# Kernel tuning notes

Measured on AMD Instinct MI355X. Metric: run time of the kernel, lower is better.

The kernel has to match this reference:

```python
import jax, jax.numpy as jnp
import numpy as np

H = 1024      # hidden_dim
E = 512       # word_emb_dim
A = 512       # av_emb_dim
L = 512       # max_length
V = 50257     # n_vocab


def setup_inputs() -> dict:
    key = jax.random.key(0)
    ks = jax.random.split(key, 16)
    s = lambda k, shape, scale=0.02: (jax.random.normal(k, shape, dtype=jnp.float32) * scale)
    return {
        "word": jax.random.randint(ks[0], (1,), 0, V),
        "enc_seq_len": 1,
        "av_emb": s(ks[1], (1, A), 1.0),
        "h0": s(ks[2], (1, 1, H), 1.0),
        "c0": s(ks[3], (1, 1, H), 1.0),
        "encoder_outputs": s(ks[4], (L, H), 1.0),
        "emb_table": s(ks[5], (V, E)),
        "attn_W": s(ks[6], (L, E + H)),
        "attn_b": s(ks[7], (L,)),
        "comb_W": s(ks[8], (H, E + H + A)),
        "comb_b": s(ks[9], (H,)),
        "W_ih": s(ks[10], (4 * H, H)),
        "W_hh": s(ks[11], (4 * H, H)),
        "b_ih": s(ks[12], (4 * H,)),
        "b_hh": s(ks[13], (4 * H,)),
        "out_W": s(ks[14], (V, H)),
        "out_b": s(ks[15], (V,)),
    }


def reference(word, enc_seq_len, av_emb, h0, c0, encoder_outputs,
              emb_table, attn_W, attn_b, comb_W, comb_b,
              W_ih, W_hh, b_ih, b_hh, out_W, out_b):
    # embedded: [1, E]
    embedded = emb_table[word].reshape(1, -1)
    h = h0[0]  # [1, H]
    c = c0[0]  # [1, H]

    # attention scores over encoder positions: [1, L]
    attn_pre = jnp.concatenate([embedded, h], axis=1) @ attn_W.T + attn_b
    # faithful to original: rows >= enc_seq_len set to -inf (no-op for batch dim of 1 when enc_seq_len>=1)
    row = jnp.arange(attn_pre.shape[0])[:, None]
    attn_pre = jnp.where(row >= enc_seq_len, -jnp.inf, attn_pre)
    attn_weights = jax.nn.softmax(attn_pre, axis=1)           # [1, L]
    attn_applied = attn_weights @ encoder_outputs             # [1, H]

    # combine + relu: [1, H]
    comb = jnp.concatenate([embedded, attn_applied, av_emb], axis=1)
    x = jax.nn.relu(comb @ comb_W.T + comb_b)

    # single-step LSTM (torch gate order: i, f, g, o)
    gates = x @ W_ih.T + b_ih + h @ W_hh.T + b_hh             # [1, 4H]
    i, f, g, o = jnp.split(gates, 4, axis=1)
    c_new = jax.nn.sigmoid(f) * c + jax.nn.sigmoid(i) * jnp.tanh(g)
    h_new = jax.nn.sigmoid(o) * jnp.tanh(c_new)

    logits = h_new @ out_W.T + out_b                          # [1, V]
    return logits, h_new[None], c_new[None], attn_weights
```

## Files before the change

### kernel.cpp

```cpp
#include <hip/hip_runtime.h>
#include <hip/hip_bf16.h>


#define WS_CAT1   0
#define WS_COMB   1536
#define WS_PRE    3584
#define WS_ATTNW  4096
#define WS_X      4608
#define WS_GATES  5632
#define WS_HNEW   9728

#define OUT_H     50257
#define OUT_C     51281
#define OUT_AW    52305

__device__ __forceinline__ float wave_partial_dot(const float* __restrict__ Wrow,
                                                  const float* __restrict__ x,
                                                  int cols) {
  int lane = threadIdx.x & 63;
  float acc = 0.f;
  for (int c = lane * 4; c < cols; c += 256) {
    float4 w  = *reinterpret_cast<const float4*>(Wrow + c);
    float4 xv = *reinterpret_cast<const float4*>(x + c);
    acc += w.x * xv.x + w.y * xv.y + w.z * xv.z + w.w * xv.w;
  }
  return acc;
}

__device__ __forceinline__ float wave_reduce(float acc) {
#pragma unroll
  for (int off = 32; off > 0; off >>= 1) acc += __shfl_xor(acc, off, 64);
  return acc;
}

__global__ __launch_bounds__(1024) void prep_k(const int* __restrict__ word,
                                               const float* __restrict__ emb_table,
                                               const float* __restrict__ h0,
                                               const float* __restrict__ av,
                                               float* __restrict__ ws) {
  int t = threadIdx.x;
  int w = word[0];
  if (t < 512) {
    float e = emb_table[(size_t)w * 512 + t];
    ws[WS_CAT1 + t] = e;
    ws[WS_COMB + t] = e;
    ws[WS_COMB + 1536 + t] = av[t];
  }
  ws[WS_CAT1 + 512 + t] = h0[t];
}

template <int COLS, bool RELU>
__global__ __launch_bounds__(256) void matvec_k(const float* __restrict__ W,
                                                const float* __restrict__ bias,
                                                const float* __restrict__ x,
                                                float* __restrict__ y,
                                                int rows) {
  int row = blockIdx.x * 4 + (threadIdx.x >> 6);
  if (row >= rows) return;
  float acc = wave_partial_dot(W + (size_t)row * COLS, x, COLS);
  acc = wave_reduce(acc);
  if ((threadIdx.x & 63) == 0) {
    acc += bias[row];
    if (RELU) acc = fmaxf(acc, 0.f);
    y[row] = acc;
  }
}

__global__ __launch_bounds__(512) void softmax_k(const float* __restrict__ pre,
                                                 float* __restrict__ wout,
                                                 float* __restrict__ out_w) {
  __shared__ float red[8];
  __shared__ float stat[2];
  int t = threadIdx.x;
  int lane = t & 63, wid = t >> 6;
  float v = pre[t];
  float m = v;
#pragma unroll
  for (int off = 32; off > 0; off >>= 1) m = fmaxf(m, __shfl_xor(m, off, 64));
  if (lane == 0) red[wid] = m;
  __syncthreads();
  if (t == 0) {
    float mm = red[0];
    for (int i = 1; i < 8; i++) mm = fmaxf(mm, red[i]);
    stat[0] = mm;
  }
  __syncthreads();
  float e = expf(v - stat[0]);
  float s = e;
#pragma unroll
  for (int off = 32; off > 0; off >>= 1) s += __shfl_xor(s, off, 64);
  if (lane == 0) red[wid] = s;
  __syncthreads();
  if (t == 0) {
    float ss = 0.f;
    for (int i = 0; i < 8; i++) ss += red[i];
    stat[1] = ss;
  }
  __syncthreads();
  float w = e / stat[1];
  wout[t] = w;
  out_w[t] = w;
}

__global__ __launch_bounds__(256) void attn_apply_k(const float* __restrict__ w,
                                                    const float* __restrict__ enc,
                                                    float* __restrict__ out) {
  int j = blockIdx.x * 256 + threadIdx.x;
  float a0 = 0.f, a1 = 0.f, a2 = 0.f, a3 = 0.f;
  for (int l = 0; l < 512; l += 4) {
    a0 += w[l + 0] * enc[(size_t)(l + 0) * 1024 + j];
    a1 += w[l + 1] * enc[(size_t)(l + 1) * 1024 + j];
    a2 += w[l + 2] * enc[(size_t)(l + 2) * 1024 + j];
    a3 += w[l + 3] * enc[(size_t)(l + 3) * 1024 + j];
  }
  out[j] = (a0 + a1) + (a2 + a3);
}

__global__ __launch_bounds__(256) void gates_k(const float* __restrict__ Wih,
                                               const float* __restrict__ Whh,
                                               const float* __restrict__ bih,
                                               const float* __restrict__ bhh,
                                               const float* __restrict__ x,
                                               const float* __restrict__ h,
                                               float* __restrict__ g) {
  int row = blockIdx.x * 4 + (threadIdx.x >> 6);
  float acc = wave_partial_dot(Wih + (size_t)row * 1024, x, 1024) +
              wave_partial_dot(Whh + (size_t)row * 1024, h, 1024);
  acc = wave_reduce(acc);
  if ((threadIdx.x & 63) == 0) g[row] = acc + bih[row] + bhh[row];
}

__global__ __launch_bounds__(1024) void lstm_k(const float* __restrict__ g,
                                               const float* __restrict__ c0,
                                               float* __restrict__ hnew_f,
                                               float* __restrict__ out_h,
                                               float* __restrict__ out_c) {
  int t = threadIdx.x;
  float gi = g[t], gf = g[1024 + t], gg = g[2048 + t], go = g[3072 + t];
  float i = 1.f / (1.f + expf(-gi));
  float f = 1.f / (1.f + expf(-gf));
  float gt = tanhf(gg);
  float o = 1.f / (1.f + expf(-go));
  float cn = f * c0[t] + i * gt;
  float hn = o * tanhf(cn);
  hnew_f[t] = hn;
  out_h[t] = hn;
  out_c[t] = cn;
}

template <int COLS>
__global__ __launch_bounds__(256) void matvec_out_k(const float* __restrict__ W,
                                                    const float* __restrict__ bias,
                                                    const float* __restrict__ x,
                                                    float* __restrict__ y,
                                                    int rows) {
  int row = blockIdx.x * 4 + (threadIdx.x >> 6);
  if (row >= rows) return;
  float acc = wave_partial_dot(W + (size_t)row * COLS, x, COLS);
  acc = wave_reduce(acc);
  if ((threadIdx.x & 63) == 0) {
    y[row] = acc + bias[row];
  }
}

extern "C" void kernel_launch(void* const* d_in, const int* in_sizes, int n_in,
                              void* d_out, int out_size, void* d_ws, size_t ws_size,
                              hipStream_t stream) {
  const int*   word   = (const int*)  d_in[0];
  const float* av     = (const float*)d_in[2];
  const float* h0     = (const float*)d_in[3];
  const float* c0     = (const float*)d_in[4];
  const float* enc    = (const float*)d_in[5];
  const float* emb    = (const float*)d_in[6];
  const float* attn_W = (const float*)d_in[7];
  const float* attn_b = (const float*)d_in[8];
  const float* comb_W = (const float*)d_in[9];
  const float* comb_b = (const float*)d_in[10];
  const float* W_ih   = (const float*)d_in[11];
  const float* W_hh   = (const float*)d_in[12];
  const float* b_ih   = (const float*)d_in[13];
  const float* b_hh   = (const float*)d_in[14];
  const float* out_W  = (const float*)d_in[15];
  const float* out_b  = (const float*)d_in[16];

  float* ws  = (float*)d_ws;
  float* out = (float*)d_out;

  prep_k<<<1, 1024, 0, stream>>>(word, emb, h0, av, ws);
  matvec_k<1536, false><<<128, 256, 0, stream>>>(attn_W, attn_b,
      ws + WS_CAT1, ws + WS_PRE, 512);
  softmax_k<<<1, 512, 0, stream>>>(ws + WS_PRE, ws + WS_ATTNW, out + OUT_AW);
  attn_apply_k<<<4, 256, 0, stream>>>(ws + WS_ATTNW, enc, ws + WS_COMB + 512);
  matvec_k<2048, true><<<256, 256, 0, stream>>>(comb_W, comb_b,
      ws + WS_COMB, ws + WS_X, 1024);
  gates_k<<<1024, 256, 0, stream>>>(W_ih, W_hh, b_ih, b_hh,
      ws + WS_X, ws + WS_CAT1 + 512, ws + WS_GATES);
  lstm_k<<<1, 1024, 0, stream>>>(ws + WS_GATES, c0,
      ws + WS_HNEW, out + OUT_H, out + OUT_C);
  matvec_out_k<1024><<<(50257 + 3) / 4, 256, 0, stream>>>(out_W, out_b,
      ws + WS_HNEW, out, 50257);
}
```

Baseline: 417.6 us.

## Fuse decoder kernels and split attention-apply over positions with atomics

Removes the prep kernel by reading the embedding row and h0 directly inside the attention and combine matvecs. The LSTM nonlinearity is fused into the gates kernel by assigning one block per hidden unit, with its four gate rows on four waves. The attention-apply step is split across 32 blocks that combine partial sums with atomics into a buffer zeroed by softmax. The logits matvec now computes two rows per wave to reuse the loaded input vector. Together these cut kernel launches and raise parallelism in the small attention-apply step, at the cost of atomic accumulation order being nondeterministic.

```diff
diff --git a/kernel.cpp b/kernel.cpp
--- a/kernel.cpp
+++ b/kernel.cpp
@@ -1,78 +1,67 @@
 #include <hip/hip_runtime.h>
-#include <hip/hip_bf16.h>
-
-
-#define WS_CAT1   0
-#define WS_COMB   1536
-#define WS_PRE    3584
-#define WS_ATTNW  4096
-#define WS_X      4608
-#define WS_GATES  5632
-#define WS_HNEW   9728
+
+
+#define V 50257
+
+#define WS_PRE    0
+#define WS_ATTNW  512
+#define WS_APPL   1024
+#define WS_X      2048
 
 #define OUT_H     50257
 #define OUT_C     51281
 #define OUT_AW    52305
 
-__device__ __forceinline__ float wave_partial_dot(const float* __restrict__ Wrow,
-                                                  const float* __restrict__ x,
-                                                  int cols) {
+__device__ __forceinline__ float4 ld4(const float* p) {
+  return *reinterpret_cast<const float4*>(p);
+}
+__device__ __forceinline__ float dot4(float4 a, float4 b) {
+  return a.x * b.x + a.y * b.y + a.z * b.z + a.w * b.w;
+}
+__device__ __forceinline__ float wave_reduce(float a) {
+#pragma unroll
+  for (int off = 32; off > 0; off >>= 1) a += __shfl_xor(a, off, 64);
+  return a;
+}
+__device__ __forceinline__ float sigf(float v) {
+  return 1.f / (1.f + expf(-v));
+}
+
+__global__ __launch_bounds__(256) void attn_mv_k(const float* __restrict__ attn_W,
+                                                 const float* __restrict__ attn_b,
+                                                 const float* __restrict__ emb,
+                                                 const int* __restrict__ word,
+                                                 const float* __restrict__ h0,
+                                                 float* __restrict__ pre) {
+  int row = blockIdx.x * 4 + (threadIdx.x >> 6);
   int lane = threadIdx.x & 63;
-  float acc = 0.f;
-  for (int c = lane * 4; c < cols; c += 256) {
-    float4 w  = *reinterpret_cast<const float4*>(Wrow + c);
-    float4 xv = *reinterpret_cast<const float4*>(x + c);
-    acc += w.x * xv.x + w.y * xv.y + w.z * xv.z + w.w * xv.w;
-  }
-  return acc;
-}
-
-__device__ __forceinline__ float wave_reduce(float acc) {
-#pragma unroll
-  for (int off = 32; off > 0; off >>= 1) acc += __shfl_xor(acc, off, 64);
-  return acc;
-}
-
-__global__ __launch_bounds__(1024) void prep_k(const int* __restrict__ word,
-                                               const float* __restrict__ emb_table,
-                                               const float* __restrict__ h0,
-                                               const float* __restrict__ av,
-                                               float* __restrict__ ws) {
-  int t = threadIdx.x;
-  int w = word[0];
-  if (t < 512) {
-    float e = emb_table[(size_t)w * 512 + t];
-    ws[WS_CAT1 + t] = e;
-    ws[WS_COMB + t] = e;
-    ws[WS_COMB + 1536 + t] = av[t];
-  }
-  ws[WS_CAT1 + 512 + t] = h0[t];
-}
-
-template <int COLS, bool RELU>
-__global__ __launch_bounds__(256) void matvec_k(const float* __restrict__ W,
-                                                const float* __restrict__ bias,
-                                                const float* __restrict__ x,
-                                                float* __restrict__ y,
-                                                int rows) {
-  int row = blockIdx.x * 4 + (threadIdx.x >> 6);
-  if (row >= rows) return;
-  float acc = wave_partial_dot(W + (size_t)row * COLS, x, COLS);
+  const float* Wr = attn_W + (size_t)row * 1536;
+  const float* er = emb + (size_t)word[0] * 512;
+  float acc = 0.f;
+#pragma unroll
+  for (int k = 0; k < 2; k++) {
+    int c = lane * 4 + k * 256;
+    acc += dot4(ld4(Wr + c), ld4(er + c));
+  }
+#pragma unroll
+  for (int k = 2; k < 6; k++) {
+    int c = lane * 4 + k * 256;
+    acc += dot4(ld4(Wr + c), ld4(h0 + c - 512));
+  }
   acc = wave_reduce(acc);
-  if ((threadIdx.x & 63) == 0) {
-    acc += bias[row];
-    if (RELU) acc = fmaxf(acc, 0.f);
-    y[row] = acc;
-  }
+  if (lane == 0) pre[row] = acc + attn_b[row];
 }
 
 __global__ __launch_bounds__(512) void softmax_k(const float* __restrict__ pre,
                                                  float* __restrict__ wout,
-                                                 float* __restrict__ out_w) {
+                                                 float* __restrict__ out_w,
+                                                 float* __restrict__ applied) {
   __shared__ float red[8];
   __shared__ float stat[2];
   int t = threadIdx.x;
   int lane = t & 63, wid = t >> 6;
+  applied[t] = 0.f;
+  applied[512 + t] = 0.f;
   float v = pre[t];
   float m = v;
 #pragma unroll
@@ -104,62 +93,106 @@
 
 __global__ __launch_bounds__(256) void attn_apply_k(const float* __restrict__ w,
                                                     const float* __restrict__ enc,
-                                                    float* __restrict__ out) {
-  int j = blockIdx.x * 256 + threadIdx.x;
-  float a0 = 0.f, a1 = 0.f, a2 = 0.f, a3 = 0.f;
-  for (int l = 0; l < 512; l += 4) {
-    a0 += w[l + 0] * enc[(size_t)(l + 0) * 1024 + j];
-    a1 += w[l + 1] * enc[(size_t)(l + 1) * 1024 + j];
-    a2 += w[l + 2] * enc[(size_t)(l + 2) * 1024 + j];
-    a3 += w[l + 3] * enc[(size_t)(l + 3) * 1024 + j];
-  }
-  out[j] = (a0 + a1) + (a2 + a3);
-}
-
-__global__ __launch_bounds__(256) void gates_k(const float* __restrict__ Wih,
-                                               const float* __restrict__ Whh,
-                                               const float* __restrict__ bih,
-                                               const float* __restrict__ bhh,
-                                               const float* __restrict__ x,
-                                               const float* __restrict__ h,
-                                               float* __restrict__ g) {
+                                                    float* __restrict__ applied) {
+  int jb = blockIdx.x & 3, lb = blockIdx.x >> 2;
+  int j = jb * 256 + threadIdx.x;
+  int l0 = lb * 64;
+  float acc = 0.f;
+#pragma unroll 4
+  for (int l = l0; l < l0 + 64; l++) acc += w[l] * enc[(size_t)l * 1024 + j];
+  atomicAdd(applied + j, acc);
+}
+
+__global__ __launch_bounds__(256) void comb_mv_k(const float* __restrict__ comb_W,
+                                                 const float* __restrict__ comb_b,
+                                                 const float* __restrict__ emb,
+                                                 const int* __restrict__ word,
+                                                 const float* __restrict__ applied,
+                                                 const float* __restrict__ av,
+                                                 float* __restrict__ x) {
   int row = blockIdx.x * 4 + (threadIdx.x >> 6);
-  float acc = wave_partial_dot(Wih + (size_t)row * 1024, x, 1024) +
-              wave_partial_dot(Whh + (size_t)row * 1024, h, 1024);
+  int lane = threadIdx.x & 63;
+  const float* Wr = comb_W + (size_t)row * 2048;
+  const float* er = emb + (size_t)word[0] * 512;
+  float acc = 0.f;
+#pragma unroll
+  for (int k = 0; k < 2; k++) {
+    int c = lane * 4 + k * 256;
+    acc += dot4(ld4(Wr + c), ld4(er + c));
+  }
+#pragma unroll
+  for (int k = 2; k < 6; k++) {
+    int c = lane * 4 + k * 256;
+    acc += dot4(ld4(Wr + c), ld4(applied + c - 512));
+  }
+#pragma unroll
+  for (int k = 6; k < 8; k++) {
+    int c = lane * 4 + k * 256;
+    acc += dot4(ld4(Wr + c), ld4(av + c - 1536));
+  }
   acc = wave_reduce(acc);
-  if ((threadIdx.x & 63) == 0) g[row] = acc + bih[row] + bhh[row];
-}
-
-__global__ __launch_bounds__(1024) void lstm_k(const float* __restrict__ g,
-                                               const float* __restrict__ c0,
-                                               float* __restrict__ hnew_f,
-                                               float* __restrict__ out_h,
-                                               float* __restrict__ out_c) {
-  int t = threadIdx.x;
-  float gi = g[t], gf = g[1024 + t], gg = g[2048 + t], go = g[3072 + t];
-  float i = 1.f / (1.f + expf(-gi));
-  float f = 1.f / (1.f + expf(-gf));
-  float gt = tanhf(gg);
-  float o = 1.f / (1.f + expf(-go));
-  float cn = f * c0[t] + i * gt;
-  float hn = o * tanhf(cn);
-  hnew_f[t] = hn;
-  out_h[t] = hn;
-  out_c[t] = cn;
-}
-
-template <int COLS>
-__global__ __launch_bounds__(256) void matvec_out_k(const float* __restrict__ W,
-                                                    const float* __restrict__ bias,
+  if (lane == 0) x[row] = fmaxf(acc + comb_b[row], 0.f);
+}
+
+__global__ __launch_bounds__(256) void gates_lstm_k(const float* __restrict__ Wih,
+                                                    const float* __restrict__ Whh,
+                                                    const float* __restrict__ bih,
+                                                    const float* __restrict__ bhh,
                                                     const float* __restrict__ x,
-                                                    float* __restrict__ y,
-                                                    int rows) {
-  int row = blockIdx.x * 4 + (threadIdx.x >> 6);
-  if (row >= rows) return;
-  float acc = wave_partial_dot(W + (size_t)row * COLS, x, COLS);
+                                                    const float* __restrict__ h0,
+                                                    const float* __restrict__ c0,
+                                                    float* __restrict__ out_h,
+                                                    float* __restrict__ out_c) {
+  __shared__ float gsh[4];
+  int t = blockIdx.x;
+  int wv = threadIdx.x >> 6, lane = threadIdx.x & 63;
+  size_t r = (size_t)wv * 1024 + t;
+  const float* Wi = Wih + r * 1024;
+  const float* Wh = Whh + r * 1024;
+  float acc = 0.f;
+#pragma unroll
+  for (int k = 0; k < 4; k++) {
+    int c = lane * 4 + k * 256;
+    acc += dot4(ld4(Wi + c), ld4(x + c));
+    acc += dot4(ld4(Wh + c), ld4(h0 + c));
+  }
   acc = wave_reduce(acc);
-  if ((threadIdx.x & 63) == 0) {
-    y[row] = acc + bias[row];
+  if (lane == 0) gsh[wv] = acc + bih[r] + bhh[r];
+  __syncthreads();
+  if (threadIdx.x == 0) {
+    float gi = sigf(gsh[0]);
+    float gf = sigf(gsh[1]);
+    float gg = tanhf(gsh[2]);
+    float go = sigf(gsh[3]);
+    float cn = gf * c0[t] + gi * gg;
+    float hn = go * tanhf(cn);
+    out_h[t] = hn;
+    out_c[t] = cn;
+  }
+}
+
+__global__ __launch_bounds__(256) void logits_mv_k(const float* __restrict__ W,
+                                                   const float* __restrict__ bias,
+                                                   const float* __restrict__ x,
+                                                   float* __restrict__ y) {
+  int wv = threadIdx.x >> 6, lane = threadIdx.x & 63;
+  int r0 = blockIdx.x * 8 + wv * 2;
+  if (r0 >= V) return;
+  bool has1 = (r0 + 1) < V;
+  const float* W0 = W + (size_t)r0 * 1024;
+  float a0 = 0.f, a1 = 0.f;
+#pragma unroll
+  for (int k = 0; k < 4; k++) {
+    int c = lane * 4 + k * 256;
+    float4 xv = ld4(x + c);
+    a0 += dot4(ld4(W0 + c), xv);
+    if (has1) a1 += dot4(ld4(W0 + 1024 + c), xv);
+  }
+  a0 = wave_reduce(a0);
+  a1 = wave_reduce(a1);
+  if (lane == 0) {
+    y[r0] = a0 + bias[r0];
+    if (has1) y[r0 + 1] = a1 + bias[r0 + 1];
   }
 }
 
@@ -186,17 +219,13 @@
   float* ws  = (float*)d_ws;
   float* out = (float*)d_out;
 
-  prep_k<<<1, 1024, 0, stream>>>(word, emb, h0, av, ws);
-  matvec_k<1536, false><<<128, 256, 0, stream>>>(attn_W, attn_b,
-      ws + WS_CAT1, ws + WS_PRE, 512);
-  softmax_k<<<1, 512, 0, stream>>>(ws + WS_PRE, ws + WS_ATTNW, out + OUT_AW);
-  attn_apply_k<<<4, 256, 0, stream>>>(ws + WS_ATTNW, enc, ws + WS_COMB + 512);
-  matvec_k<2048, true><<<256, 256, 0, stream>>>(comb_W, comb_b,
-      ws + WS_COMB, ws + WS_X, 1024);
-  gates_k<<<1024, 256, 0, stream>>>(W_ih, W_hh, b_ih, b_hh,
-      ws + WS_X, ws + WS_CAT1 + 512, ws + WS_GATES);
-  lstm_k<<<1, 1024, 0, stream>>>(ws + WS_GATES, c0,
-      ws + WS_HNEW, out + OUT_H, out + OUT_C);
-  matvec_out_k<1024><<<(50257 + 3) / 4, 256, 0, stream>>>(out_W, out_b,
-      ws + WS_HNEW, out, 50257);
-}
+  attn_mv_k<<<128, 256, 0, stream>>>(attn_W, attn_b, emb, word, h0, ws + WS_PRE);
+  softmax_k<<<1, 512, 0, stream>>>(ws + WS_PRE, ws + WS_ATTNW, out + OUT_AW,
+                                   ws + WS_APPL);
+  attn_apply_k<<<32, 256, 0, stream>>>(ws + WS_ATTNW, enc, ws + WS_APPL);
+  comb_mv_k<<<256, 256, 0, stream>>>(comb_W, comb_b, emb, word, ws + WS_APPL,
+                                     av, ws + WS_X);
+  gates_lstm_k<<<1024, 256, 0, stream>>>(W_ih, W_hh, b_ih, b_hh, ws + WS_X,
+                                         h0, c0, out + OUT_H, out + OUT_C);
+  logits_mv_k<<<(V + 7) / 8, 256, 0, stream>>>(out_W, out_b, out + OUT_H, out);
+}
```

New measurement: 395.6 us. 5.3% less time.
